# Optimization experiments

Measured on AMD Instinct MI355X. Metric: run time of the kernel, lower is better.

Reference implementation:

```python
import jax, jax.numpy as jnp
import numpy as np

TOP_K = 8
N_GROUP = 8
TOPK_GROUP = 4


def setup_inputs() -> dict:
    key = jax.random.key(0)
    k1, k2, k3 = jax.random.split(key, 3)
    T, H, E = 16384, 4096, 256
    x = jax.random.normal(k1, (T, H), dtype=jnp.float32)
    gate_w = jax.random.normal(k2, (E, H), dtype=jnp.float32) * 0.02
    correction_bias = jax.random.normal(k3, (E,), dtype=jnp.float32) * 0.01
    return {"x": x, "gate_w": gate_w, "correction_bias": correction_bias}


def reference(x, gate_w, correction_bias):
    # gate linear (no bias), computed in float32
    raw_logits = jnp.einsum('th,eh->te', x, gate_w).astype(jnp.float32)  # (T, E)
    logits = jax.nn.sigmoid(raw_logits)
    z_loss = jnp.mean(jnp.square(raw_logits))

    sel = logits + correction_bias  # bias-corrected selection scores

    T, E = sel.shape
    epg = E // N_GROUP  # experts per group
    grouped = sel.reshape(T, N_GROUP, epg)
    # group score = sum of top-2 expert scores in the group
    group_scores = jax.lax.top_k(grouped, 2)[0].sum(axis=-1)          # (T, n_group)
    top_groups = jax.lax.top_k(group_scores, TOPK_GROUP)[1]           # (T, topk_group)
    group_mask = jnp.zeros((T, N_GROUP), dtype=sel.dtype).at[
        jnp.arange(T)[:, None], top_groups].set(1.0)                  # (T, n_group)
    expert_mask = jnp.repeat(group_mask, epg, axis=1)                 # (T, E)
    neg = jnp.finfo(sel.dtype).min
    sel = jnp.where(expert_mask == 0, neg, sel)

    _, indices = jax.lax.top_k(sel, TOP_K)                            # (T, top_k)
    # combine weights come from raw sigmoid scores (bias-free), renormalized
    weights = jnp.take_along_axis(logits, indices, axis=-1)
    weights = weights / jnp.clip(weights.sum(axis=-1, keepdims=True), 1e-9)
    return (weights, indices, z_loss, logits)
```

## Files before the change

kernel.cpp:

```cpp
#include <hip/hip_runtime.h>
#include <math.h>

#define TT 16384
#define HH 4096
#define EE 256

typedef _Float16 f16x8 __attribute__((ext_vector_type(8)));
typedef float f32x4 __attribute__((ext_vector_type(4)));

__device__ inline void atom_add_double(double* addr, double val) {
    unsigned long long* p = (unsigned long long*)addr;
    unsigned long long old = *p, assumed;
    do {
        assumed = old;
        double nv = __longlong_as_double(assumed) + val;
        old = atomicCAS(p, assumed, __double_as_longlong(nv));
    } while (old != assumed);
}

__global__ __launch_bounds__(64) void zero_ws_kernel(double* z) {
    if (threadIdx.x == 0) *z = 0.0;
}

__global__ __launch_bounds__(64) void finalize_z_kernel(const double* zacc,
                                                        float* zout) {
    if (threadIdx.x == 0)
        *zout = (float)(*zacc / (double)((size_t)TT * (size_t)EE));
}

__global__ __launch_bounds__(256) void finalize_zpart_kernel(
    const double* __restrict__ zpart, float* __restrict__ zout) {
    __shared__ double zr[256];
    zr[threadIdx.x] = zpart[threadIdx.x] + zpart[threadIdx.x + 256];
    __syncthreads();
    for (int s = 128; s > 0; s >>= 1) {
        if (threadIdx.x < s) zr[threadIdx.x] += zr[threadIdx.x + s];
        __syncthreads();
    }
    if (threadIdx.x == 0)
        *zout = (float)(zr[0] / ((double)TT * (double)EE));
}

__global__ __launch_bounds__(256) void prep_w_kernel(
    const float* __restrict__ w, _Float16* __restrict__ wpl)
{
    const int e = blockIdx.x;
    for (int c = threadIdx.x; c < 512; c += 256) {
        const int k = c << 3;
        const float* src = w + (size_t)e * HH + k;
        const float4 f0 = *(const float4*)src;
        const float4 f1 = *(const float4*)(src + 4);
        const float fs[8] = {f0.x, f0.y, f0.z, f0.w, f1.x, f1.y, f1.z, f1.w};
        f16x8 hi, lo;
#pragma unroll
        for (int q = 0; q < 8; ++q) {
            _Float16 h = (_Float16)fs[q];
            hi[q] = h;
            lo[q] = (_Float16)((fs[q] - (float)h) * 2048.0f);
        }
        *(f16x8*)(wpl + (size_t)e * HH + k) = hi;
        *(f16x8*)(wpl + (size_t)EE * HH + (size_t)e * HH + k) = lo;
    }
}

__global__ __launch_bounds__(512, 4) void gemm_mfma_kernel(
    const float* __restrict__ x,
    const _Float16* __restrict__ wpl,
    float* __restrict__ logits,
    double* __restrict__ zpart)
{
    __shared__ __align__(16) unsigned char sm[2][16384];
    __shared__ float zred[8];

    const int tid  = threadIdx.x;
    const int lane = tid & 63;
    const int wid  = tid >> 6;
    const int wm   = wid >> 2;
    const int wn   = wid & 3;
    const int lr   = lane & 15;
    const int lc   = lane >> 4;

    const int bid  = blockIdx.x;
    const int rb   = ((bid & 7) << 5) + (bid >> 4);
    const int cb   = (bid >> 3) & 1;
    const int row0 = rb << 6;
    const int col0 = cb << 7;

    const int arow = tid >> 2, ac32 = tid & 3;
    const float* aSrc = x + (size_t)(row0 + arow) * HH + (ac32 << 3);
    const int aDst = (arow << 6) + ((ac32 ^ ((arow >> 1) & 3)) << 4);

    const int br = tid >> 2, bc4 = tid & 3;
    const _Float16* bhiSrc = wpl + (size_t)(col0 + br) * HH + (bc4 << 3);
    const int bhiDst = 8192 + (br << 6) + ((bc4 ^ ((br >> 1) & 3)) << 4);

    const _Float16* bloSrc[2];
#pragma unroll
    for (int j = 0; j < 2; ++j)
        bloSrc[j] = wpl + (size_t)EE * HH +
                    (size_t)(col0 + (wn << 5) + (j << 4) + lr) * HH + (lc << 3);

    int aRd[2], bRd[2];
#pragma unroll
    for (int i = 0; i < 2; ++i) {
        const int r = (wm << 5) + (i << 4) + lr;
        aRd[i] = (r << 6) + ((lc ^ ((r >> 1) & 3)) << 4);
    }
#pragma unroll
    for (int j = 0; j < 2; ++j) {
        const int r = (wn << 5) + (j << 4) + lr;
        bRd[j] = 8192 + (r << 6) + ((lc ^ ((r >> 1) & 3)) << 4);
    }

    f32x4 accP[2][2] = {};
    f32x4 accS[2][2] = {};
    float4 Aa0, Aa1, Ab0, Ab1;
    uint4 h0;
    f16x8 Pa[2], Pb[2];

#define CVT_STORE_A(SMW, X0, X1)                                              \
    if (tid < 256) {                                                          \
        const float fs[8] = {X0.x, X0.y, X0.z, X0.w, X1.x, X1.y, X1.z, X1.w}; \
        f16x8 hi, lo;                                                         \
        _Pragma("unroll") for (int q = 0; q < 8; ++q)                         \
        {                                                                     \
            _Float16 hv = (_Float16)fs[q];                                    \
            hi[q] = hv;                                                       \
            lo[q] = (_Float16)((fs[q] - (float)hv) * 2048.0f);                \
        }                                                                     \
        *(f16x8*)((SMW) + aDst) = hi;                                         \
        *(f16x8*)((SMW) + 4096 + aDst) = lo;                                  \
    }

#define BODY(T, CUR, X0, X1, Y0, Y1, PUSE, PLD)                               \
    {                                                                         \
        if ((T) < 126 && tid < 256) {                                         \
            const float* ap = aSrc + (size_t)((T) + 2) * 32;                  \
            Y0 = *(const float4*)ap;                                          \
            Y1 = *(const float4*)(ap + 4);                                    \
        }                                                                     \
        if ((T) < 127) {                                                      \
            h0 = *(const uint4*)(bhiSrc + (size_t)((T) + 1) * 32);            \
            _Pragma("unroll") for (int j = 0; j < 2; ++j)                     \
                PLD[j] = *(const f16x8*)(bloSrc[j] + (size_t)((T) + 1) * 32); \
        }                                                                     \
        const unsigned char* sb = sm[CUR];                                    \
        f16x8 ahh[2], ahl[2], bhh[2];                                         \
        _Pragma("unroll") for (int i = 0; i < 2; ++i)                         \
        {                                                                     \
            ahh[i] = *(const f16x8*)(sb + aRd[i]);                            \
            ahl[i] = *(const f16x8*)(sb + 4096 + aRd[i]);                     \
        }                                                                     \
        _Pragma("unroll") for (int j = 0; j < 2; ++j)                         \
            bhh[j] = *(const f16x8*)(sb + bRd[j]);                            \
        _Pragma("unroll") for (int i = 0; i < 2; ++i)                         \
            _Pragma("unroll") for (int j = 0; j < 2; ++j)                     \
        {                                                                     \
            accP[i][j] = __builtin_amdgcn_mfma_f32_16x16x32_f16(              \
                ahh[i], bhh[j], accP[i][j], 0, 0, 0);                         \
            accS[i][j] = __builtin_amdgcn_mfma_f32_16x16x32_f16(              \
                ahh[i], PUSE[j], accS[i][j], 0, 0, 0);                        \
            accS[i][j] = __builtin_amdgcn_mfma_f32_16x16x32_f16(              \
                ahl[i], bhh[j], accS[i][j], 0, 0, 0);                         \
        }                                                                     \
        if ((T) < 127) {                                                      \
            unsigned char* smw = sm[1 - (CUR)];                               \
            CVT_STORE_A(smw, X0, X1);                                         \
            *(uint4*)(smw + bhiDst) = h0;                                     \
            asm volatile("s_waitcnt lgkmcnt(0)" ::: "memory");                \
            __builtin_amdgcn_s_barrier();                                     \
        }                                                                     \
    }

    if (tid < 256) {
        Aa0 = *(const float4*)aSrc;
        Aa1 = *(const float4*)(aSrc + 4);
    }
    h0 = *(const uint4*)bhiSrc;
#pragma unroll
    for (int j = 0; j < 2; ++j) Pa[j] = *(const f16x8*)bloSrc[j];
    {
        unsigned char* smw = sm[0];
        CVT_STORE_A(smw, Aa0, Aa1);
        *(uint4*)(smw + bhiDst) = h0;
    }
    if (tid < 256) {
        const float* ap = aSrc + 32;
        Aa0 = *(const float4*)ap;
        Aa1 = *(const float4*)(ap + 4);
    }
    asm volatile("s_waitcnt lgkmcnt(0)" ::: "memory");
    __builtin_amdgcn_s_barrier();

    for (int t = 0; t < 128; t += 2) {
        BODY(t,     0, Aa0, Aa1, Ab0, Ab1, Pa, Pb);
        BODY(t + 1, 1, Ab0, Ab1, Aa0, Aa1, Pb, Pa);
    }
#undef BODY
#undef CVT_STORE_A

    float zs = 0.f;
#pragma unroll
    for (int i = 0; i < 2; ++i) {
        const int rb0 = row0 + (wm << 5) + (i << 4) + (lc << 2);
#pragma unroll
        for (int j = 0; j < 2; ++j) {
            const int col = col0 + (wn << 5) + (j << 4) + lr;
#pragma unroll
            for (int r = 0; r < 4; ++r) {
                const float raw =
                    accP[i][j][r] + accS[i][j][r] * 4.8828125e-4f;
                zs = fmaf(raw, raw, zs);
                logits[(size_t)(rb0 + r) * EE + col] =
                    1.f / (1.f + expf(-raw));
            }
        }
    }
#pragma unroll
    for (int d = 32; d; d >>= 1) zs += __shfl_xor(zs, d);
    if (lane == 0) zred[wid] = zs;
    __syncthreads();
    if (tid == 0) {
        double zt = 0.0;
#pragma unroll
        for (int q = 0; q < 8; ++q) zt += (double)zred[q];
        zpart[bid] = zt;
    }
}

#define BM 32
#define BK 32
__global__ __launch_bounds__(256) void gemm_fp32_fb_kernel(
    const float* __restrict__ x, const float* __restrict__ w,
    float* __restrict__ logits, double* __restrict__ zacc)
{
    __shared__ float As[BM][BK + 1];
    __shared__ float Bs[EE][BK + 1];
    __shared__ float zred[256];

    const int tid = threadIdx.x;
    const int row0 = blockIdx.x * BM;
    const int ty = tid >> 5;
    const int tx = tid & 31;
    const int lrow = tid >> 3;
    const int lk = (tid & 7) << 2;

    float acc[4][8];
#pragma unroll
    for (int i = 0; i < 4; ++i)
#pragma unroll
        for (int j = 0; j < 8; ++j) acc[i][j] = 0.f;

    for (int k0 = 0; k0 < HH; k0 += BK) {
        float4 xa = *(const float4*)(x + (size_t)(row0 + lrow) * HH + k0 + lk);
        As[lrow][lk + 0] = xa.x;
        As[lrow][lk + 1] = xa.y;
        As[lrow][lk + 2] = xa.z;
        As[lrow][lk + 3] = xa.w;
#pragma unroll
        for (int j = 0; j < 8; ++j) {
            const int e = lrow + (j << 5);
            float4 wb = *(const float4*)(w + (size_t)e * HH + k0 + lk);
            Bs[e][lk + 0] = wb.x;
            Bs[e][lk + 1] = wb.y;
            Bs[e][lk + 2] = wb.z;
            Bs[e][lk + 3] = wb.w;
        }
        __syncthreads();
#pragma unroll 8
        for (int kk = 0; kk < BK; ++kk) {
            float a[4], bb[8];
#pragma unroll
            for (int i = 0; i < 4; ++i) a[i] = As[ty * 4 + i][kk];
#pragma unroll
            for (int j = 0; j < 8; ++j) bb[j] = Bs[tx + (j << 5)][kk];
#pragma unroll
            for (int i = 0; i < 4; ++i)
#pragma unroll
                for (int j = 0; j < 8; ++j)
                    acc[i][j] = fmaf(a[i], bb[j], acc[i][j]);
        }
        __syncthreads();
    }

    float zs = 0.f;
#pragma unroll
    for (int i = 0; i < 4; ++i) {
        const int r = row0 + ty * 4 + i;
#pragma unroll
        for (int j = 0; j < 8; ++j) {
            const float v = acc[i][j];
            zs = fmaf(v, v, zs);
            logits[(size_t)r * EE + tx + (j << 5)] = 1.f / (1.f + expf(-v));
        }
    }
    zred[tid] = zs;
    __syncthreads();
    for (int s = 128; s > 0; s >>= 1) {
        if (tid < s) zred[tid] += zred[tid + s];
        __syncthreads();
    }
    if (tid == 0) atom_add_double(zacc, (double)zred[0]);
}

__global__ __launch_bounds__(256) void router_kernel(
    const float* __restrict__ logits, const float* __restrict__ bias,
    float* __restrict__ wout, float* __restrict__ iout)
{
    const int lane = threadIdx.x & 63;
    const int wv = threadIdx.x >> 6;
    const int t = blockIdx.x * 4 + wv;

    const float* lrow = logits + (size_t)t * EE + lane * 4;
    float lg[4];
#pragma unroll
    for (int q = 0; q < 4; ++q) lg[q] = lrow[q];
    const float4 b4 = *(const float4*)(bias + lane * 4);
    const float bb[4] = {b4.x, b4.y, b4.z, b4.w};

    float sel[4];
#pragma unroll
    for (int q = 0; q < 4; ++q) sel[q] = lg[q] + bb[q];

    float m1 = sel[0], m2 = -INFINITY;
#pragma unroll
    for (int q = 1; q < 4; ++q) {
        if (sel[q] > m1) { m2 = m1; m1 = sel[q]; }
        else             { m2 = fmaxf(m2, sel[q]); }
    }
#pragma unroll
    for (int d = 1; d < 8; d <<= 1) {
        const float o1 = __shfl_xor(m1, d);
        const float o2 = __shfl_xor(m2, d);
        const float nm1 = fmaxf(m1, o1);
        const float nm2 = fmaxf(fminf(m1, o1), fmaxf(m2, o2));
        m1 = nm1; m2 = nm2;
    }
    const float gs = m1 + m2;
    const int g = lane >> 3;

    int rank = 0;
#pragma unroll
    for (int gp = 0; gp < 8; ++gp) {
        const float og = __shfl(gs, gp << 3);
        rank += (og > gs) || (og == gs && gp < g);
    }
    const bool keep = rank < 4;

    float ms[4];
#pragma unroll
    for (int q = 0; q < 4; ++q)
        ms[q] = keep ? sel[q] : -3.402823466e38f;

    float wvals[8];
    int widx[8];
#pragma unroll
    for (int it = 0; it < 8; ++it) {
        float bv = ms[0];
        int bq = 0;
#pragma unroll
        for (int q = 1; q < 4; ++q)
            if (ms[q] > bv) { bv = ms[q]; bq = q; }
        int bi = (lane << 2) + bq;
        float bl = lg[bq];
#pragma unroll
        for (int d = 1; d < 64; d <<= 1) {
            const float ov = __shfl_xor(bv, d);
            const int oi = __shfl_xor(bi, d);
            const float ol = __shfl_xor(bl, d);
            if (ov > bv || (ov == bv && oi < bi)) { bv = ov; bi = oi; bl = ol; }
        }
        wvals[it] = bl;
        widx[it] = bi;
        if ((bi >> 2) == lane) ms[bi & 3] = -INFINITY;
    }

    float s = 0.f;
#pragma unroll
    for (int it = 0; it < 8; ++it) s += wvals[it];
    s = fmaxf(s, 1e-9f);

    if (lane == 0) {
#pragma unroll
        for (int it = 0; it < 8; ++it) {
            wout[(size_t)t * 8 + it] = wvals[it] / s;
            iout[(size_t)t * 8 + it] = (float)widx[it];
        }
    }
}

extern "C" void kernel_launch(void* const* d_in, const int* in_sizes, int n_in,
                              void* d_out, int out_size, void* d_ws,
                              size_t ws_size, hipStream_t stream) {
    const float* x = (const float*)d_in[0];
    const float* w = (const float*)d_in[1];
    const float* bias = (const float*)d_in[2];

    float* out = (float*)d_out;
    float* wout = out;
    float* iout = out + (size_t)TT * 8;
    float* zout = out + (size_t)TT * 16;
    float* logits = zout + 1;
    double* zacc = (double*)d_ws;

    const size_t need = 8192 + (size_t)2 * EE * HH * sizeof(_Float16);
    if (ws_size >= need) {
        double* zpart = (double*)((char*)d_ws + 1024);
        _Float16* wpl = (_Float16*)((char*)d_ws + 8192);
        prep_w_kernel<<<EE, 256, 0, stream>>>(w, wpl);
        gemm_mfma_kernel<<<(TT / 64) * 2, 512, 0, stream>>>(x, wpl, logits,
                                                            zpart);
        finalize_zpart_kernel<<<1, 256, 0, stream>>>(zpart, zout);
    } else {
        zero_ws_kernel<<<1, 64, 0, stream>>>(zacc);
        gemm_fp32_fb_kernel<<<TT / BM, 256, 0, stream>>>(x, w, logits, zacc);
        finalize_z_kernel<<<1, 64, 0, stream>>>(zacc, zout);
    }
    router_kernel<<<TT / 4, 256, 0, stream>>>(logits, bias, wout, iout);
}
```

Baseline: 547.8 us.

## Double K-tile depth to 64 per stage and raise MFMA wave priority

Each pipeline stage of the split-fp16 MFMA GEMM now covers 64 K elements instead of 32. Shared memory per buffer doubles, the XOR swizzle is widened to 8 chunks, and all 512 threads take part in loading and converting A. This halves the number of barriers and loop iterations and gives each thread more bytes in flight per load. s_setprio is raised around the MFMA section to favour compute waves. The cost is 64KB of LDS and more registers, which may reduce occupancy from the 4-blocks launch bound.

```diff
diff --git a/kernel.cpp b/kernel.cpp
--- a/kernel.cpp
+++ b/kernel.cpp
@@ -69,7 +69,7 @@
     float* __restrict__ logits,
     double* __restrict__ zpart)
 {
-    __shared__ __align__(16) unsigned char sm[2][16384];
+    __shared__ __align__(16) unsigned char sm[2][32768];
     __shared__ float zred[8];
 
     const int tid  = threadIdx.x;
@@ -86,13 +86,15 @@
     const int row0 = rb << 6;
     const int col0 = cb << 7;
 
-    const int arow = tid >> 2, ac32 = tid & 3;
-    const float* aSrc = x + (size_t)(row0 + arow) * HH + (ac32 << 3);
-    const int aDst = (arow << 6) + ((ac32 ^ ((arow >> 1) & 3)) << 4);
-
-    const int br = tid >> 2, bc4 = tid & 3;
-    const _Float16* bhiSrc = wpl + (size_t)(col0 + br) * HH + (bc4 << 3);
-    const int bhiDst = 8192 + (br << 6) + ((bc4 ^ ((br >> 1) & 3)) << 4);
+    const int arow = tid >> 3, ach = tid & 7;
+    const float* aSrc = x + (size_t)(row0 + arow) * HH + (ach << 3);
+    const int aDst = (arow << 7) + ((ach ^ (arow & 7)) << 4);
+
+    const int br = tid >> 3, bch = tid & 7;
+    const _Float16* bhiSrc0 = wpl + (size_t)(col0 + br) * HH + (bch << 3);
+    const _Float16* bhiSrc1 = bhiSrc0 + (size_t)64 * HH;
+    const int bhiDst0 = 16384 + (br << 7) + ((bch ^ (br & 7)) << 4);
+    const int bhiDst1 = bhiDst0 + 8192;
 
     const _Float16* bloSrc[2];
 #pragma unroll
@@ -100,26 +102,30 @@
         bloSrc[j] = wpl + (size_t)EE * HH +
                     (size_t)(col0 + (wn << 5) + (j << 4) + lr) * HH + (lc << 3);
 
-    int aRd[2], bRd[2];
+    int aRd[2][2], bRd[2][2];
 #pragma unroll
     for (int i = 0; i < 2; ++i) {
         const int r = (wm << 5) + (i << 4) + lr;
-        aRd[i] = (r << 6) + ((lc ^ ((r >> 1) & 3)) << 4);
+#pragma unroll
+        for (int ks = 0; ks < 2; ++ks)
+            aRd[i][ks] = (r << 7) + ((((ks << 2) + lc) ^ (r & 7)) << 4);
     }
 #pragma unroll
     for (int j = 0; j < 2; ++j) {
         const int r = (wn << 5) + (j << 4) + lr;
-        bRd[j] = 8192 + (r << 6) + ((lc ^ ((r >> 1) & 3)) << 4);
+#pragma unroll
+        for (int ks = 0; ks < 2; ++ks)
+            bRd[j][ks] = 16384 + (r << 7) + ((((ks << 2) + lc) ^ (r & 7)) << 4);
     }
 
     f32x4 accP[2][2] = {};
     f32x4 accS[2][2] = {};
     float4 Aa0, Aa1, Ab0, Ab1;
-    uint4 h0;
-    f16x8 Pa[2], Pb[2];
+    uint4 h0, h1;
+    f16x8 Pa[4], Pb[4];
 
 #define CVT_STORE_A(SMW, X0, X1)                                              \
-    if (tid < 256) {                                                          \
+    {                                                                         \
         const float fs[8] = {X0.x, X0.y, X0.z, X0.w, X1.x, X1.y, X1.z, X1.w}; \
         f16x8 hi, lo;                                                         \
         _Pragma("unroll") for (int q = 0; q < 8; ++q)                         \
@@ -129,70 +135,82 @@
             lo[q] = (_Float16)((fs[q] - (float)hv) * 2048.0f);                \
         }                                                                     \
         *(f16x8*)((SMW) + aDst) = hi;                                         \
-        *(f16x8*)((SMW) + 4096 + aDst) = lo;                                  \
+        *(f16x8*)((SMW) + 8192 + aDst) = lo;                                  \
     }
 
 #define BODY(T, CUR, X0, X1, Y0, Y1, PUSE, PLD)                               \
     {                                                                         \
-        if ((T) < 126 && tid < 256) {                                         \
-            const float* ap = aSrc + (size_t)((T) + 2) * 32;                  \
+        if ((T) < 62) {                                                       \
+            const float* ap = aSrc + (size_t)((T) + 2) * 64;                  \
             Y0 = *(const float4*)ap;                                          \
             Y1 = *(const float4*)(ap + 4);                                    \
         }                                                                     \
-        if ((T) < 127) {                                                      \
-            h0 = *(const uint4*)(bhiSrc + (size_t)((T) + 1) * 32);            \
+        if ((T) < 63) {                                                       \
+            h0 = *(const uint4*)(bhiSrc0 + (size_t)((T) + 1) * 64);           \
+            h1 = *(const uint4*)(bhiSrc1 + (size_t)((T) + 1) * 64);           \
             _Pragma("unroll") for (int j = 0; j < 2; ++j)                     \
-                PLD[j] = *(const f16x8*)(bloSrc[j] + (size_t)((T) + 1) * 32); \
+                _Pragma("unroll") for (int ks = 0; ks < 2; ++ks)              \
+                PLD[(j << 1) + ks] = *(const f16x8*)(                         \
+                    bloSrc[j] + (size_t)((T) + 1) * 64 + (ks << 5));          \
         }                                                                     \
         const unsigned char* sb = sm[CUR];                                    \
-        f16x8 ahh[2], ahl[2], bhh[2];                                         \
-        _Pragma("unroll") for (int i = 0; i < 2; ++i)                         \
+        __builtin_amdgcn_s_setprio(1);                                        \
+        _Pragma("unroll") for (int ks = 0; ks < 2; ++ks)                      \
         {                                                                     \
-            ahh[i] = *(const f16x8*)(sb + aRd[i]);                            \
-            ahl[i] = *(const f16x8*)(sb + 4096 + aRd[i]);                     \
+            f16x8 ahh[2], ahl[2], bhh[2];                                     \
+            _Pragma("unroll") for (int i = 0; i < 2; ++i)                     \
+            {                                                                 \
+                ahh[i] = *(const f16x8*)(sb + aRd[i][ks]);                    \
+                ahl[i] = *(const f16x8*)(sb + 8192 + aRd[i][ks]);             \
+            }                                                                 \
+            _Pragma("unroll") for (int j = 0; j < 2; ++j)                     \
+                bhh[j] = *(const f16x8*)(sb + bRd[j][ks]);                    \
+            _Pragma("unroll") for (int i = 0; i < 2; ++i)                     \
+                _Pragma("unroll") for (int j = 0; j < 2; ++j)                 \
+            {                                                                 \
+                accP[i][j] = __builtin_amdgcn_mfma_f32_16x16x32_f16(          \
+                    ahh[i], bhh[j], accP[i][j], 0, 0, 0);                     \
+                accS[i][j] = __builtin_amdgcn_mfma_f32_16x16x32_f16(          \
+                    ahh[i], PUSE[(j << 1) + ks], accS[i][j], 0, 0, 0);        \
+                accS[i][j] = __builtin_amdgcn_mfma_f32_16x16x32_f16(          \
+                    ahl[i], bhh[j], accS[i][j], 0, 0, 0);                     \
+            }                                                                 \
         }                                                                     \
-        _Pragma("unroll") for (int j = 0; j < 2; ++j)                         \
-            bhh[j] = *(const f16x8*)(sb + bRd[j]);                            \
-        _Pragma("unroll") for (int i = 0; i < 2; ++i)                         \
-            _Pragma("unroll") for (int j = 0; j < 2; ++j)                     \
-        {                                                                     \
-            accP[i][j] = __builtin_amdgcn_mfma_f32_16x16x32_f16(              \
-                ahh[i], bhh[j], accP[i][j], 0, 0, 0);                         \
-            accS[i][j] = __builtin_amdgcn_mfma_f32_16x16x32_f16(              \
-                ahh[i], PUSE[j], accS[i][j], 0, 0, 0);                        \
-            accS[i][j] = __builtin_amdgcn_mfma_f32_16x16x32_f16(              \
-                ahl[i], bhh[j], accS[i][j], 0, 0, 0);                         \
-        }                                                                     \
-        if ((T) < 127) {                                                      \
+        __builtin_amdgcn_s_setprio(0);                                        \
+        if ((T) < 63) {                                                       \
             unsigned char* smw = sm[1 - (CUR)];                               \
             CVT_STORE_A(smw, X0, X1);                                         \
-            *(uint4*)(smw + bhiDst) = h0;                                     \
+            *(uint4*)(smw + bhiDst0) = h0;                                    \
+            *(uint4*)(smw + bhiDst1) = h1;                                    \
             asm volatile("s_waitcnt lgkmcnt(0)" ::: "memory");                \
             __builtin_amdgcn_s_barrier();                                     \
         }                                                                     \
     }
 
-    if (tid < 256) {
-        Aa0 = *(const float4*)aSrc;
-        Aa1 = *(const float4*)(aSrc + 4);
-    }
-    h0 = *(const uint4*)bhiSrc;
-#pragma unroll
-    for (int j = 0; j < 2; ++j) Pa[j] = *(const f16x8*)bloSrc[j];
+    Aa0 = *(const float4*)aSrc;
+    Aa1 = *(const float4*)(aSrc + 4);
+    h0 = *(const uint4*)bhiSrc0;
+    h1 = *(const uint4*)bhiSrc1;
+#pragma unroll
+    for (int j = 0; j < 2; ++j)
+#pragma unroll
+        for (int ks = 0; ks < 2; ++ks)
+            Pa[(j << 1) + ks] = *(const f16x8*)(bloSrc[j] + (ks << 5));
     {
         unsigned char* smw = sm[0];
         CVT_STORE_A(smw, Aa0, Aa1);
-        *(uint4*)(smw + bhiDst) = h0;
-    }
-    if (tid < 256) {
-        const float* ap = aSrc + 32;
+        *(uint4*)(smw + bhiDst0) = h0;
+        *(uint4*)(smw + bhiDst1) = h1;
+    }
+    {
+        const float* ap = aSrc + 64;
         Aa0 = *(const float4*)ap;
         Aa1 = *(const float4*)(ap + 4);
     }
     asm volatile("s_waitcnt lgkmcnt(0)" ::: "memory");
     __builtin_amdgcn_s_barrier();
 
-    for (int t = 0; t < 128; t += 2) {
+    for (int t = 0; t < 64; t += 2) {
         BODY(t,     0, Aa0, Aa1, Ab0, Ab1, Pa, Pb);
         BODY(t + 1, 1, Ab0, Ab1, Aa0, Aa1, Pb, Pa);
     }
```

After: 566.0 us. +3.3%, slower.
